# Performance work log

Measured on AMD Instinct MI355X. Metric: run time of the kernel, lower is better.

The kernel has to match this reference:

```python
import jax, jax.numpy as jnp
import numpy as np

NEG_SLOPE = 0.2  # PyG GATConv default negative_slope
HEADS1, HID = 8, 256


def gat_conv(x, src, dst, W, att_src, att_dst, bias, heads, out_ch):
    """PyG-style GATConv: project, per-edge attention, segment softmax over dst, scatter-add."""
    N = x.shape[0]
    h = (x @ W.T).reshape(N, heads, out_ch)                 # [N,H,C]
    a_s = jnp.einsum('nhc,hc->nh', h, att_src)              # [N,H]
    a_d = jnp.einsum('nhc,hc->nh', h, att_dst)
    e = jax.nn.leaky_relu(a_s[src] + a_d[dst], NEG_SLOPE)   # [E,H]
    m = jax.ops.segment_max(e, dst, num_segments=N)         # stable softmax per dst node
    ex = jnp.exp(e - m[dst])
    denom = jax.ops.segment_sum(ex, dst, num_segments=N)
    alpha = ex / (denom[dst] + 1e-16)                       # [E,H]
    out = jax.ops.segment_sum(alpha[:, :, None] * h[src], dst, num_segments=N)  # [N,H,C]
    return out.reshape(N, heads * out_ch) + bias


def setup_inputs() -> dict:
    key = jax.random.key(0)
    ks = jax.random.split(key, 20)
    Nc, Ncol, E = 4000, 16000, 100000
    nf, cf, gain, hid, H, emb = 64, 128, 2, HID, HEADS1, 128
    s = 0.05
    return {
        'constraints_state': jax.random.normal(ks[0], (Nc, nf), jnp.float32),
        'columns_state':     jax.random.normal(ks[1], (Ncol, cf), jnp.float32),
        'edges':             jax.random.randint(ks[2], (2, E), 0, Nc + Ncol, jnp.int64),
        'W_node': jax.random.normal(ks[3], (hid, nf * gain), jnp.float32) * s,
        'b_node': jnp.zeros((hid,), jnp.float32),
        'W_col':  jax.random.normal(ks[4], (hid, cf * gain), jnp.float32) * s,
        'b_col':  jnp.zeros((hid,), jnp.float32),
        'W1':       jax.random.normal(ks[5], (H * hid, hid), jnp.float32) * s,
        'att_src1': jax.random.normal(ks[6], (H, hid), jnp.float32) * s,
        'att_dst1': jax.random.normal(ks[7], (H, hid), jnp.float32) * s,
        'b1':       jnp.zeros((H * hid,), jnp.float32),
        'W2':       jax.random.normal(ks[8], (hid, H * hid), jnp.float32) * s,
        'att_src2': jax.random.normal(ks[9], (1, hid), jnp.float32) * s,
        'att_dst2': jax.random.normal(ks[10], (1, hid), jnp.float32) * s,
        'b2':       jnp.zeros((hid,), jnp.float32),
        'W_out': jax.random.normal(ks[11], (emb, hid), jnp.float32) * s,
        'b_out': jnp.zeros((emb,), jnp.float32),
    }


def reference(constraints_state, columns_state, edges,
              W_node, b_node, W_col, b_col,
              W1, att_src1, att_dst1, b1,
              W2, att_src2, att_dst2, b2,
              W_out, b_out):
    gain = 2
    x_n = jnp.tile(constraints_state, (1, gain))
    x_c = jnp.tile(columns_state, (1, gain))
    h_n = jax.nn.relu(x_n @ W_node.T + b_node)
    h_c = jax.nn.relu(x_c @ W_col.T + b_col)
    x = jnp.concatenate([h_n, h_c], axis=0)                 # [N, hid]
    N = x.shape[0]
    loops = jnp.arange(N)
    # conv1: edges as given (+ self-loops, PyG default)
    src1 = jnp.concatenate([edges[0], loops])
    dst1 = jnp.concatenate([edges[1], loops])
    x = jax.nn.relu(gat_conv(x, src1, dst1, W1, att_src1, att_dst1, b1, HEADS1, HID))
    # conv2: flipped edges (+ self-loops), 1 head
    src2 = jnp.concatenate([edges[1], loops])
    dst2 = jnp.concatenate([edges[0], loops])
    x = jax.nn.relu(gat_conv(x, src2, dst2, W2, att_src2, att_dst2, b2, 1, HID))
    logits = x[-columns_state.shape[0]:] @ W_out.T + b_out  # [Ncol, embed_dim]
    return logits
```

## Files before the change

### kernel.cpp

```cpp
#include <hip/hip_runtime.h>


#define NEG_SLOPE 0.2f

typedef __attribute__((ext_vector_type(8))) short bf16x8;
typedef __attribute__((ext_vector_type(4))) float f32x4;

__device__ __forceinline__ float bf2f(unsigned short u) {
  return __uint_as_float(((unsigned)u) << 16);
}
__device__ __forceinline__ unsigned short f2bf(float f) {
  unsigned u = __float_as_uint(f);
  u += 0x7fffu + ((u >> 16) & 1u);
  return (unsigned short)(u >> 16);
}

__device__ __forceinline__ void async_copy16(const void* g, void* l) {
  __builtin_amdgcn_global_load_lds(
      (const __attribute__((address_space(1))) unsigned int*)g,
      (__attribute__((address_space(3))) unsigned int*)l, 16, 0, 0);
}

__global__ void prep(const float* __restrict__ Wn, const float* __restrict__ Wc,
                     const float* __restrict__ W1, const float* __restrict__ W2,
                     const float* __restrict__ Wout,
                     const float* __restrict__ cons, const float* __restrict__ cols,
                     const float* __restrict__ att_s1, const float* __restrict__ att_d1,
                     unsigned short* __restrict__ Wn_b, unsigned short* __restrict__ Wc_b,
                     unsigned short* __restrict__ W1b, unsigned short* __restrict__ W2b,
                     unsigned short* __restrict__ Woutb,
                     unsigned short* __restrict__ consb, unsigned short* __restrict__ colsb,
                     float* __restrict__ v_s1, float* __restrict__ v_d1,
                     int n_cons, int n_cols) {
  const int S0 = 256 * 64;
  const int S1 = 256 * 128;
  const int S2 = 2048 * 256;
  const int S3 = 256 * 2048;
  const int S4 = 128 * 256;
  const int S5 = 2048;
  int total = S0 + S1 + S2 + S3 + S4 + n_cons + n_cols + S5;
  for (int idx = blockIdx.x * 256 + threadIdx.x; idx < total; idx += gridDim.x * 256) {
    int i = idx;
    if (i < S0) { int o = i >> 6, j = i & 63;
      Wn_b[i] = f2bf(Wn[o * 128 + j] + Wn[o * 128 + 64 + j]); continue; }
    i -= S0;
    if (i < S1) { int o = i >> 7, j = i & 127;
      Wc_b[i] = f2bf(Wc[o * 256 + j] + Wc[o * 256 + 128 + j]); continue; }
    i -= S1;
    if (i < S2) { W1b[i] = f2bf(W1[i]); continue; }
    i -= S2;
    if (i < S3) { W2b[i] = f2bf(W2[i]); continue; }
    i -= S3;
    if (i < S4) { Woutb[i] = f2bf(Wout[i]); continue; }
    i -= S4;
    if (i < n_cons) { consb[i] = f2bf(cons[i]); continue; }
    i -= n_cons;
    if (i < n_cols) { colsb[i] = f2bf(cols[i]); continue; }
    i -= n_cols;
    {
      int h = i >> 8, k = i & 255;
      const float* Wrow = W1 + (size_t)h * 256 * 256 + k;
      const float* as = att_s1 + h * 256;
      const float* ad = att_d1 + h * 256;
      float s = 0.f, d = 0.f;
      for (int c = 0; c < 256; ++c) {
        float w = Wrow[(size_t)c * 256];
        s += as[c] * w;
        d += ad[c] * w;
      }
      v_s1[i] = s; v_d1[i] = d;
    }
  }
}

__global__ __launch_bounds__(256) void a1_dots(const unsigned short* __restrict__ xb,
                                               const float* __restrict__ v_s,
                                               const float* __restrict__ v_d,
                                               float* __restrict__ a_s,
                                               float* __restrict__ a_d, int N) {
  __shared__ float vs[2048], vd[2048];
  for (int i = threadIdx.x; i < 2048; i += 256) { vs[i] = v_s[i]; vd[i] = v_d[i]; }
  __syncthreads();
  int n = blockIdx.x * 256 + threadIdx.x;
  if (n >= N) return;
  const unsigned short* row = xb + (size_t)n * 256;
  float s[8] = {}, d[8] = {};
  for (int c = 0; c < 256; c += 8) {
    bf16x8 xv = *(const bf16x8*)(row + c);
    float xf[8];
#pragma unroll
    for (int i = 0; i < 8; ++i) xf[i] = bf2f(((const unsigned short*)&xv)[i]);
#pragma unroll
    for (int h = 0; h < 8; ++h)
#pragma unroll
      for (int i = 0; i < 8; ++i) {
        s[h] += xf[i] * vs[h * 256 + c + i];
        d[h] += xf[i] * vd[h * 256 + c + i];
      }
  }
#pragma unroll
  for (int h = 0; h < 8; ++h) { a_s[n * 8 + h] = s[h]; a_d[n * 8 + h] = d[h]; }
}

__global__ __launch_bounds__(256) void a2_dots(const unsigned short* __restrict__ h2,
                                               const float* __restrict__ att_s,
                                               const float* __restrict__ att_d,
                                               float* __restrict__ a_s,
                                               float* __restrict__ a_d, int N) {
  __shared__ float ss[256], sd[256];
  if (threadIdx.x < 256) {
    ss[threadIdx.x] = att_s[threadIdx.x];
    sd[threadIdx.x] = att_d[threadIdx.x];
  }
  __syncthreads();
  int n = blockIdx.x * 256 + threadIdx.x;
  if (n >= N) return;
  const unsigned short* row = h2 + (size_t)n * 256;
  float s = 0.f, d = 0.f;
  for (int c = 0; c < 256; c += 8) {
    bf16x8 xv = *(const bf16x8*)(row + c);
#pragma unroll
    for (int i = 0; i < 8; ++i) {
      float hv = bf2f(((const unsigned short*)&xv)[i]);
      s += hv * ss[c + i];
      d += hv * sd[c + i];
    }
  }
  a_s[n] = s;
  a_d[n] = d;
}

template <bool C_BF16, bool BIAS, bool RELU, bool BDIAG, bool SWZ>
__global__ __launch_bounds__(512) void gemm_mfma_bt(const unsigned short* __restrict__ A,
                                                    const unsigned short* __restrict__ W,
                                                    const float* __restrict__ bias,
                                                    void* __restrict__ Cv,
                                                    int M, int K, int Nout, int lda) {
  __shared__ short smem[2 * 128 * 64];
  short* sA = smem;
  short* sB = smem + 128 * 64;
  float* Cf = (float*)Cv;
  unsigned short* Cb = (unsigned short*)Cv;

  const int tid = threadIdx.x;
  const int lane = tid & 63, w = tid >> 6;

  const int gx = gridDim.x;
  int wg = blockIdx.y * gx + blockIdx.x;
  if (SWZ) {
    const int nwg = gx * gridDim.y;
    int orig = wg;
    int q = nwg >> 3, r = nwg & 7;
    int xcd = orig & 7, idx = orig >> 3;
    wg = (xcd < r ? xcd * (q + 1) : r * (q + 1) + (xcd - r) * q) + idx;
  }
  const int m0 = (wg / gx) * 128, n0 = (wg % gx) * 128;

  const int koff = BDIAG ? (n0 >> 8) << 8 : 0;
  const int wm = (w & 3) * 32, wn = (w >> 2) * 64;
  const int fr = lane & 15;
  const int frs = fr & 7;
  const int quad = lane >> 4;

  f32x4 acc[2][4];
#pragma unroll
  for (int i = 0; i < 2; ++i)
#pragma unroll
    for (int j = 0; j < 4; ++j) acc[i][j] = (f32x4){0.f, 0.f, 0.f, 0.f};

  for (int k0 = 0; k0 < K; k0 += 64) {
#pragma unroll
    for (int i = 0; i < 2; ++i) {
      int c = i * 512 + tid;
      int row = c >> 3, kc = c & 7;
      int kcs = kc ^ (row & 7);
      int grow = m0 + row;
      if (grow >= M) grow = M - 1;
      async_copy16(A + (size_t)grow * lda + koff + k0 + kcs * 8, &sA[(i * 512 + w * 64) * 8]);
    }
#pragma unroll
    for (int i = 0; i < 2; ++i) {
      int c = i * 512 + tid;
      int row = c >> 3, kc = c & 7;
      int kcs = kc ^ (row & 7);
      async_copy16(W + (size_t)(n0 + row) * K + k0 + kcs * 8, &sB[(i * 512 + w * 64) * 8]);
    }
    __syncthreads();

#pragma unroll
    for (int ks = 0; ks < 2; ++ks) {
      bf16x8 af[2], bfr[4];
#pragma unroll
      for (int mi = 0; mi < 2; ++mi) {
        int row = wm + mi * 16 + fr;
        af[mi] = *(const bf16x8*)&sA[(row * 8 + ((ks * 4 + quad) ^ frs)) * 8];
      }
#pragma unroll
      for (int ni = 0; ni < 4; ++ni) {
        int row = wn + ni * 16 + fr;
        bfr[ni] = *(const bf16x8*)&sB[(row * 8 + ((ks * 4 + quad) ^ frs)) * 8];
      }
#pragma unroll
      for (int mi = 0; mi < 2; ++mi)
#pragma unroll
        for (int ni = 0; ni < 4; ++ni)
          acc[mi][ni] = __builtin_amdgcn_mfma_f32_16x16x32_bf16(
              af[mi], bfr[ni], acc[mi][ni], 0, 0, 0);
    }
    __syncthreads();
  }

  if (C_BF16) {
    unsigned short* hsh = (unsigned short*)smem;
#pragma unroll
    for (int mi = 0; mi < 2; ++mi)
#pragma unroll
      for (int ni = 0; ni < 4; ++ni) {
        int col = wn + ni * 16 + fr;
        float bv = BIAS ? bias[n0 + col] : 0.f;
        f32x4 v = acc[mi][ni];
#pragma unroll
        for (int r = 0; r < 4; ++r) {
          int row = wm + mi * 16 + quad * 4 + r;
          float x = v[r] + bv;
          if (RELU) x = fmaxf(x, 0.f);
          hsh[row * 128 + (col ^ (((row >> 2) & 3) << 5))] = f2bf(x);
        }
      }
    __syncthreads();
#pragma unroll
    for (int i = 0; i < 4; ++i) {
      int slot = i * 512 + tid;
      int row = slot >> 4, cg = slot & 15;
      int colbase = cg * 8;
      bf16x8 val = *(const bf16x8*)&hsh[row * 128 + (colbase ^ (((row >> 2) & 3) << 5))];
      int grow = m0 + row;
      if (grow < M)
        *(bf16x8*)(Cb + (size_t)grow * Nout + n0 + colbase) = val;
    }
  } else {
#pragma unroll
    for (int mi = 0; mi < 2; ++mi)
#pragma unroll
      for (int ni = 0; ni < 4; ++ni) {
        int col = n0 + wn + ni * 16 + fr;
        float bv = BIAS ? bias[col] : 0.f;
        f32x4 v = acc[mi][ni];
#pragma unroll
        for (int r = 0; r < 4; ++r) {
          int row = m0 + wm + mi * 16 + quad * 4 + r;
          if (row < M) {
            float x = v[r] + bv;
            if (RELU) x = fmaxf(x, 0.f);
            Cf[(size_t)row * Nout + col] = x;
          }
        }
      }
  }
}

__global__ void build_count(const void* __restrict__ edges_raw, int E, int N,
                            int* __restrict__ esrc, int* __restrict__ edst,
                            int* __restrict__ cnt1, int* __restrict__ cnt2, int E1) {
  const long long* p64 = (const long long*)edges_raw;
  const int* p32 = (const int*)edges_raw;
  bool is64 = true;
#pragma unroll
  for (int i = 0; i < 8; ++i) {
    long long v = p64[i];
    if (v < 0 || v >= N) is64 = false;
  }
  int idx = blockIdx.x * 256 + threadIdx.x;
  if (idx >= E1) return;
  int s, d;
  if (idx < E) {
    if (is64) { s = (int)p64[idx]; d = (int)p64[E + idx]; }
    else      { s = p32[idx];      d = p32[E + idx]; }
  } else {
    s = d = idx - E;
  }
  esrc[idx] = s;
  edst[idx] = d;
  atomicAdd(&cnt1[d], 1);
  atomicAdd(&cnt2[s], 1);
}

__device__ __forceinline__ void scan_one(const int* __restrict__ cnt,
                                         int* __restrict__ indptr,
                                         int* __restrict__ cur, int N, int* buf) {
  int t = threadIdx.x, lane = t & 63, w = t >> 6;
  int running = 0;
  for (int base = 0; base < N; base += 1024) {
    int v = (base + t < N) ? cnt[base + t] : 0;
    int incl = v;
#pragma unroll
    for (int off = 1; off < 64; off <<= 1) {
      int y = __shfl_up(incl, off);
      if (lane >= off) incl += y;
    }
    if (lane == 63) buf[w] = incl;
    __syncthreads();
    if (t < 16) {
      int x = buf[t];
#pragma unroll
      for (int off = 1; off < 16; off <<= 1) {
        int y = __shfl_up(x, off);
        if (t >= off) x += y;
      }
      buf[t] = x;
    }
    __syncthreads();
    int woff = w ? buf[w - 1] : 0;
    int tot = buf[15];
    if (base + t < N) {
      int excl = running + woff + incl - v;
      indptr[base + t] = excl;
      cur[base + t] = excl;
    }
    running += tot;
    __syncthreads();
  }
  if (t == 0) indptr[N] = running;
  __syncthreads();
}

__global__ __launch_bounds__(1024) void scan2_kernel(const int* cnt1, int* indptr1, int* cur1,
                                                     const int* cnt2, int* indptr2, int* cur2,
                                                     int N) {
  __shared__ int buf[16];
  if (blockIdx.x == 0) scan_one(cnt1, indptr1, cur1, N, buf);
  else                 scan_one(cnt2, indptr2, cur2, N, buf);
}

__global__ void scatter_edges(const int* __restrict__ esrc, const int* __restrict__ edst,
                              int* __restrict__ cur1, int* __restrict__ cur2,
                              int* __restrict__ nbr1, int* __restrict__ nbr2, int E1) {
  int e = blockIdx.x * 256 + threadIdx.x;
  if (e >= E1) return;
  int s = esrc[e], d = edst[e];
  int p1 = atomicAdd(&cur1[d], 1);
  nbr1[p1] = s;
  int p2 = atomicAdd(&cur2[s], 1);
  nbr2[p2] = d;
}

__global__ __launch_bounds__(256) void agg1_fused(const unsigned short* __restrict__ xb,
                                                  const float* __restrict__ a_s,
                                                  const float* __restrict__ a_d,
                                                  const int* __restrict__ indptr,
                                                  const int* __restrict__ nbr,
                                                  unsigned short* __restrict__ agg,
                                                  int N) {
  __shared__ float al_sh[4][64 * 8];
  const int w = threadIdx.x >> 6, lane = threadIdx.x & 63;
  const int dst = blockIdx.x * 4 + w;
  if (dst >= N) return;
  const int start = indptr[dst];
  const int deg = indptr[dst + 1] - start;
  const int c0 = lane * 4;

  float ad[8];
  *(float4*)&ad[0] = *(const float4*)&a_d[dst * 8];
  *(float4*)&ad[4] = *(const float4*)&a_d[dst * 8 + 4];

  float psum[8];
#pragma unroll
  for (int h = 0; h < 8; ++h) psum[h] = 0.f;

  float acc[8][4];
#pragma unroll
  for (int h = 0; h < 8; ++h)
#pragma unroll
    for (int i = 0; i < 4; ++i) acc[h][i] = 0.f;

  for (int base = 0; base < deg; base += 64) {
    int cnt = min(64, deg - base);
    int s = 0;
    if (lane < cnt) {
      s = nbr[start + base + lane];
      float as[8];
      *(float4*)&as[0] = *(const float4*)&a_s[s * 8];
      *(float4*)&as[4] = *(const float4*)&a_s[s * 8 + 4];
      float p8[8];
#pragma unroll
      for (int h = 0; h < 8; ++h) {
        float e = as[h] + ad[h];
        e = e > 0.f ? e : NEG_SLOPE * e;
        float pv = __expf(e);
        p8[h] = pv;
        psum[h] += pv;
      }
#pragma unroll
      for (int h = 0; h < 8; ++h) al_sh[w][lane * 8 + h] = p8[h];
    }
    __builtin_amdgcn_wave_barrier();
    for (int j = 0; j < cnt; ++j) {
      int sj = __shfl(s, j);
      f32x4 alo = *(const f32x4*)&al_sh[w][j * 8];
      f32x4 ahi = *(const f32x4*)&al_sh[w][j * 8 + 4];
      ushort4 xv = *(const ushort4*)(xb + (size_t)sj * 256 + c0);
      float x0 = bf2f(xv.x), x1 = bf2f(xv.y), x2 = bf2f(xv.z), x3 = bf2f(xv.w);
#pragma unroll
      for (int h = 0; h < 4; ++h) {
        acc[h][0] += alo[h] * x0; acc[h][1] += alo[h] * x1;
        acc[h][2] += alo[h] * x2; acc[h][3] += alo[h] * x3;
      }
#pragma unroll
      for (int h = 0; h < 4; ++h) {
        acc[h + 4][0] += ahi[h] * x0; acc[h + 4][1] += ahi[h] * x1;
        acc[h + 4][2] += ahi[h] * x2; acc[h + 4][3] += ahi[h] * x3;
      }
    }
    __builtin_amdgcn_wave_barrier();
  }

  float inv[8];
#pragma unroll
  for (int h = 0; h < 8; ++h) {
    float t = psum[h];
#pragma unroll
    for (int off = 32; off; off >>= 1) t += __shfl_xor(t, off);
    inv[h] = 1.f / (t + 1e-16f);
  }

  unsigned short* op = agg + (size_t)dst * 2048;
#pragma unroll
  for (int h = 0; h < 8; ++h) {
    unsigned short ov[4];
#pragma unroll
    for (int i = 0; i < 4; ++i) ov[i] = f2bf(acc[h][i] * inv[h]);
    *((ushort4*)(op + h * 256 + c0)) = *((const ushort4*)ov);
  }
}

__global__ __launch_bounds__(256) void agg2_fused(const unsigned short* __restrict__ h2,
                                                  const float* __restrict__ a_s,
                                                  const float* __restrict__ a_d,
                                                  const int* __restrict__ indptr,
                                                  const int* __restrict__ nbr,
                                                  const float* __restrict__ b2,
                                                  unsigned short* __restrict__ x3,
                                                  int Nc, int Ncol) {
  const int w = threadIdx.x >> 6, lane = threadIdx.x & 63;
  const int i0 = blockIdx.x * 4 + w;
  if (i0 >= Ncol) return;
  const int dst = Nc + i0;
  const int start = indptr[dst];
  const int deg = indptr[dst + 1] - start;
  const float ad = a_d[dst];
  float psum = 0.f;
  float acc[4] = {0.f, 0.f, 0.f, 0.f};
  const int c0 = lane * 4;

  for (int base = 0; base < deg; base += 64) {
    int cnt = min(64, deg - base);
    int s = 0;
    float p = 0.f;
    if (lane < cnt) {
      s = nbr[start + base + lane];
      float e = a_s[s] + ad;
      e = e > 0.f ? e : NEG_SLOPE * e;
      p = __expf(e);
      psum += p;
    }
    for (int j = 0; j < cnt; ++j) {
      int sj = __shfl(s, j);
      float al = __shfl(p, j);
      ushort4 hv = *(const ushort4*)(h2 + (size_t)sj * 256 + c0);
      acc[0] += al * bf2f(hv.x);
      acc[1] += al * bf2f(hv.y);
      acc[2] += al * bf2f(hv.z);
      acc[3] += al * bf2f(hv.w);
    }
  }

  float t = psum;
#pragma unroll
  for (int off = 32; off; off >>= 1) t += __shfl_xor(t, off);
  float inv = 1.f / (t + 1e-16f);

  float4 bv = *(const float4*)&b2[c0];
  unsigned short ov[4];
  ov[0] = f2bf(fmaxf(acc[0] * inv + bv.x, 0.f));
  ov[1] = f2bf(fmaxf(acc[1] * inv + bv.y, 0.f));
  ov[2] = f2bf(fmaxf(acc[2] * inv + bv.z, 0.f));
  ov[3] = f2bf(fmaxf(acc[3] * inv + bv.w, 0.f));
  *((ushort4*)(x3 + (size_t)i0 * 256 + c0)) = *((const ushort4*)ov);
}

extern "C" void kernel_launch(void* const* d_in, const int* in_sizes, int n_in,
                              void* d_out, int out_size, void* d_ws, size_t ws_size,
                              hipStream_t stream) {
  (void)n_in; (void)out_size; (void)ws_size;
  const float* constraints = (const float*)d_in[0];
  const float* columns     = (const float*)d_in[1];
  const void*  edges       = d_in[2];
  const float* W_node = (const float*)d_in[3];
  const float* b_node = (const float*)d_in[4];
  const float* W_col  = (const float*)d_in[5];
  const float* b_col  = (const float*)d_in[6];
  const float* W1       = (const float*)d_in[7];
  const float* att_src1 = (const float*)d_in[8];
  const float* att_dst1 = (const float*)d_in[9];
  const float* b1       = (const float*)d_in[10];
  const float* W2       = (const float*)d_in[11];
  const float* att_src2 = (const float*)d_in[12];
  const float* att_dst2 = (const float*)d_in[13];
  const float* b2       = (const float*)d_in[14];
  const float* W_out    = (const float*)d_in[15];
  const float* b_out    = (const float*)d_in[16];

  const int Nc   = in_sizes[0] / 64;
  const int Ncol = in_sizes[1] / 128;
  const int E    = in_sizes[2] / 2;
  const int N    = Nc + Ncol;
  const int E1   = E + N;

  char* p = (char*)d_ws;
  size_t off = 0;
  auto alloc = [&](size_t nbytes) -> void* {
    void* r = p + off;
    off = (off + nbytes + 255) & ~(size_t)255;
    return r;
  };
  unsigned short* Wn_b  = (unsigned short*)alloc(2ull * 256 * 64);
  unsigned short* Wc_b  = (unsigned short*)alloc(2ull * 256 * 128);
  unsigned short* W1b   = (unsigned short*)alloc(2ull * 2048 * 256);
  unsigned short* W2b   = (unsigned short*)alloc(2ull * 256 * 2048);
  unsigned short* Woutb = (unsigned short*)alloc(2ull * 128 * 256);
  unsigned short* consb = (unsigned short*)alloc(2ull * (size_t)Nc * 64);
  unsigned short* colsb = (unsigned short*)alloc(2ull * (size_t)Ncol * 128);
  unsigned short* xb    = (unsigned short*)alloc(2ull * (size_t)N * 256);
  float* v_s1 = (float*)alloc(sizeof(float) * 8 * 256);
  float* v_d1 = (float*)alloc(sizeof(float) * 8 * 256);
  float* a_s1 = (float*)alloc(sizeof(float) * (size_t)N * 8);
  float* a_d1 = (float*)alloc(sizeof(float) * (size_t)N * 8);
  int* esrc = (int*)alloc(4ull * E1);
  int* edst = (int*)alloc(4ull * E1);
  int* cnt1 = (int*)alloc(4ull * 2 * N);
  int* cnt2 = cnt1 + N;
  int* indptr1 = (int*)alloc(4ull * (N + 1));
  int* cur1    = (int*)alloc(4ull * N);
  int* indptr2 = (int*)alloc(4ull * (N + 1));
  int* cur2    = (int*)alloc(4ull * N);
  int* nbr1 = (int*)alloc(4ull * E1);
  int* nbr2 = (int*)alloc(4ull * E1);
  unsigned short* agg = (unsigned short*)alloc(2ull * (size_t)N * 2048);
  unsigned short* x2  = (unsigned short*)alloc(2ull * (size_t)N * 2048);
  unsigned short* h2b = (unsigned short*)alloc(2ull * (size_t)N * 256);
  float* a_s2 = (float*)alloc(sizeof(float) * (size_t)N);
  float* a_d2 = (float*)alloc(sizeof(float) * (size_t)N);
  unsigned short* x3 = (unsigned short*)alloc(2ull * (size_t)Ncol * 256);

  hipMemsetAsync(cnt1, 0, 4ull * 2 * N, stream);
  prep<<<1024, 256, 0, stream>>>(W_node, W_col, W1, W2, W_out, constraints, columns,
                                 att_src1, att_dst1,
                                 Wn_b, Wc_b, W1b, W2b, Woutb, consb, colsb,
                                 v_s1, v_d1, Nc * 64, Ncol * 128);

  gemm_mfma_bt<true, true, true, false, false><<<dim3(2, (Nc + 127) / 128), 512, 0, stream>>>(
      consb, Wn_b, b_node, xb, Nc, 64, 256, 64);
  gemm_mfma_bt<true, true, true, false, false><<<dim3(2, (Ncol + 127) / 128), 512, 0, stream>>>(
      colsb, Wc_b, b_col, xb + (size_t)Nc * 256, Ncol, 128, 256, 128);

  a1_dots<<<(N + 255) / 256, 256, 0, stream>>>(xb, v_s1, v_d1, a_s1, a_d1, N);

  build_count<<<(E1 + 255) / 256, 256, 0, stream>>>(edges, E, N, esrc, edst, cnt1, cnt2, E1);
  scan2_kernel<<<2, 1024, 0, stream>>>(cnt1, indptr1, cur1, cnt2, indptr2, cur2, N);
  scatter_edges<<<(E1 + 255) / 256, 256, 0, stream>>>(esrc, edst, cur1, cur2, nbr1, nbr2, E1);

  agg1_fused<<<(N + 3) / 4, 256, 0, stream>>>(xb, a_s1, a_d1, indptr1, nbr1, agg, N);
  gemm_mfma_bt<true, true, true, true, true><<<dim3(16, (N + 127) / 128), 512, 0, stream>>>(
      agg, W1b, b1, x2, N, 256, 2048, 2048);

  gemm_mfma_bt<true, false, false, false, false><<<dim3(2, (N + 127) / 128), 512, 0, stream>>>(
      x2, W2b, nullptr, h2b, N, 2048, 256, 2048);
  a2_dots<<<(N + 255) / 256, 256, 0, stream>>>(h2b, att_src2, att_dst2, a_s2, a_d2, N);
  agg2_fused<<<(Ncol + 3) / 4, 256, 0, stream>>>(h2b, a_s2, a_d2, indptr2, nbr2, b2, x3,
                                                 Nc, Ncol);

  gemm_mfma_bt<false, true, false, false, false><<<dim3(1, (Ncol + 127) / 128), 512, 0, stream>>>(
      x3, Woutb, b_out, (float*)d_out, Ncol, 256, 128, 256);
}
```

Measured before the change: 339.0 us.

## Split-K the conv2 projection GEMM with fp32 atomics and fuse bf16 conversion

The conv2 projection GEMM (K=2048, output width 256) launched only 2x157 workgroups. It now splits K four ways across blockIdx.z and atomically adds fp32 partials into a zeroed buffer. The zeroing is folded into the existing memset, and a2_dots now reads the fp32 result, writes the bf16 copy, and computes the attention dots from the rounded values. This trades more parallelism on a long-K GEMM for fp32 atomic traffic, a larger memset, and non-deterministic summation order.

```diff
diff --git a/kernel.cpp b/kernel.cpp
--- a/kernel.cpp
+++ b/kernel.cpp
@@ -102,7 +102,8 @@
   for (int h = 0; h < 8; ++h) { a_s[n * 8 + h] = s[h]; a_d[n * 8 + h] = d[h]; }
 }
 
-__global__ __launch_bounds__(256) void a2_dots(const unsigned short* __restrict__ h2,
+__global__ __launch_bounds__(256) void a2_dots(const float* __restrict__ h2f,
+                                               unsigned short* __restrict__ h2b,
                                                const float* __restrict__ att_s,
                                                const float* __restrict__ att_d,
                                                float* __restrict__ a_s,
@@ -115,22 +116,24 @@
   __syncthreads();
   int n = blockIdx.x * 256 + threadIdx.x;
   if (n >= N) return;
-  const unsigned short* row = h2 + (size_t)n * 256;
+  const float* row = h2f + (size_t)n * 256;
+  unsigned short* orow = h2b + (size_t)n * 256;
   float s = 0.f, d = 0.f;
-  for (int c = 0; c < 256; c += 8) {
-    bf16x8 xv = *(const bf16x8*)(row + c);
-#pragma unroll
-    for (int i = 0; i < 8; ++i) {
-      float hv = bf2f(((const unsigned short*)&xv)[i]);
-      s += hv * ss[c + i];
-      d += hv * sd[c + i];
-    }
+  for (int c = 0; c < 256; c += 4) {
+    float4 xv = *(const float4*)(row + c);
+    unsigned short ov[4];
+    ov[0] = f2bf(xv.x); ov[1] = f2bf(xv.y); ov[2] = f2bf(xv.z); ov[3] = f2bf(xv.w);
+    *(ushort4*)(orow + c) = *(const ushort4*)ov;
+    s += bf2f(ov[0]) * ss[c] + bf2f(ov[1]) * ss[c + 1] +
+         bf2f(ov[2]) * ss[c + 2] + bf2f(ov[3]) * ss[c + 3];
+    d += bf2f(ov[0]) * sd[c] + bf2f(ov[1]) * sd[c + 1] +
+         bf2f(ov[2]) * sd[c + 2] + bf2f(ov[3]) * sd[c + 3];
   }
   a_s[n] = s;
   a_d[n] = d;
 }
 
-template <bool C_BF16, bool BIAS, bool RELU, bool BDIAG, bool SWZ>
+template <bool C_BF16, bool BIAS, bool RELU, bool BDIAG, bool SWZ, int SK>
 __global__ __launch_bounds__(512) void gemm_mfma_bt(const unsigned short* __restrict__ A,
                                                     const unsigned short* __restrict__ W,
                                                     const float* __restrict__ bias,
@@ -157,6 +160,8 @@
   const int m0 = (wg / gx) * 128, n0 = (wg % gx) * 128;
 
   const int koff = BDIAG ? (n0 >> 8) << 8 : 0;
+  const int kspan = K / SK;
+  const int kbeg = (SK > 1) ? blockIdx.z * kspan : 0;
   const int wm = (w & 3) * 32, wn = (w >> 2) * 64;
   const int fr = lane & 15;
   const int frs = fr & 7;
@@ -168,7 +173,7 @@
 #pragma unroll
     for (int j = 0; j < 4; ++j) acc[i][j] = (f32x4){0.f, 0.f, 0.f, 0.f};
 
-  for (int k0 = 0; k0 < K; k0 += 64) {
+  for (int k0 = kbeg; k0 < kbeg + kspan; k0 += 64) {
 #pragma unroll
     for (int i = 0; i < 2; ++i) {
       int c = i * 512 + tid;
@@ -250,9 +255,13 @@
         for (int r = 0; r < 4; ++r) {
           int row = m0 + wm + mi * 16 + quad * 4 + r;
           if (row < M) {
-            float x = v[r] + bv;
-            if (RELU) x = fmaxf(x, 0.f);
-            Cf[(size_t)row * Nout + col] = x;
+            if (SK > 1) {
+              atomicAdd(&Cf[(size_t)row * Nout + col], v[r]);
+            } else {
+              float x = v[r] + bv;
+              if (RELU) x = fmaxf(x, 0.f);
+              Cf[(size_t)row * Nout + col] = x;
+            }
           }
         }
       }
@@ -535,10 +544,15 @@
   float* v_d1 = (float*)alloc(sizeof(float) * 8 * 256);
   float* a_s1 = (float*)alloc(sizeof(float) * (size_t)N * 8);
   float* a_d1 = (float*)alloc(sizeof(float) * (size_t)N * 8);
+
+  size_t zoff0 = off;
+  int* cnt1 = (int*)alloc(4ull * 2 * N);
+  int* cnt2 = cnt1 + N;
+  float* h2f = (float*)alloc(sizeof(float) * (size_t)N * 256);
+  size_t zbytes = off - zoff0;
+
   int* esrc = (int*)alloc(4ull * E1);
   int* edst = (int*)alloc(4ull * E1);
-  int* cnt1 = (int*)alloc(4ull * 2 * N);
-  int* cnt2 = cnt1 + N;
   int* indptr1 = (int*)alloc(4ull * (N + 1));
   int* cur1    = (int*)alloc(4ull * N);
   int* indptr2 = (int*)alloc(4ull * (N + 1));
@@ -552,15 +566,15 @@
   float* a_d2 = (float*)alloc(sizeof(float) * (size_t)N);
   unsigned short* x3 = (unsigned short*)alloc(2ull * (size_t)Ncol * 256);
 
-  hipMemsetAsync(cnt1, 0, 4ull * 2 * N, stream);
+  hipMemsetAsync(cnt1, 0, zbytes, stream);
   prep<<<1024, 256, 0, stream>>>(W_node, W_col, W1, W2, W_out, constraints, columns,
                                  att_src1, att_dst1,
                                  Wn_b, Wc_b, W1b, W2b, Woutb, consb, colsb,
                                  v_s1, v_d1, Nc * 64, Ncol * 128);
 
-  gemm_mfma_bt<true, true, true, false, false><<<dim3(2, (Nc + 127) / 128), 512, 0, stream>>>(
+  gemm_mfma_bt<true, true, true, false, false, 1><<<dim3(2, (Nc + 127) / 128), 512, 0, stream>>>(
       consb, Wn_b, b_node, xb, Nc, 64, 256, 64);
-  gemm_mfma_bt<true, true, true, false, false><<<dim3(2, (Ncol + 127) / 128), 512, 0, stream>>>(
+  gemm_mfma_bt<true, true, true, false, false, 1><<<dim3(2, (Ncol + 127) / 128), 512, 0, stream>>>(
       colsb, Wc_b, b_col, xb + (size_t)Nc * 256, Ncol, 128, 256, 128);
 
   a1_dots<<<(N + 255) / 256, 256, 0, stream>>>(xb, v_s1, v_d1, a_s1, a_d1, N);
@@ -570,15 +584,15 @@
   scatter_edges<<<(E1 + 255) / 256, 256, 0, stream>>>(esrc, edst, cur1, cur2, nbr1, nbr2, E1);
 
   agg1_fused<<<(N + 3) / 4, 256, 0, stream>>>(xb, a_s1, a_d1, indptr1, nbr1, agg, N);
-  gemm_mfma_bt<true, true, true, true, true><<<dim3(16, (N + 127) / 128), 512, 0, stream>>>(
+  gemm_mfma_bt<true, true, true, true, true, 1><<<dim3(16, (N + 127) / 128), 512, 0, stream>>>(
       agg, W1b, b1, x2, N, 256, 2048, 2048);
 
-  gemm_mfma_bt<true, false, false, false, false><<<dim3(2, (N + 127) / 128), 512, 0, stream>>>(
-      x2, W2b, nullptr, h2b, N, 2048, 256, 2048);
-  a2_dots<<<(N + 255) / 256, 256, 0, stream>>>(h2b, att_src2, att_dst2, a_s2, a_d2, N);
+  gemm_mfma_bt<false, false, false, false, false, 4><<<dim3(2, (N + 127) / 128, 4), 512, 0, stream>>>(
+      x2, W2b, nullptr, h2f, N, 2048, 256, 2048);
+  a2_dots<<<(N + 255) / 256, 256, 0, stream>>>(h2f, h2b, att_src2, att_dst2, a_s2, a_d2, N);
   agg2_fused<<<(Ncol + 3) / 4, 256, 0, stream>>>(h2b, a_s2, a_d2, indptr2, nbr2, b2, x3,
                                                  Nc, Ncol);
 
-  gemm_mfma_bt<false, true, false, false, false><<<dim3(1, (Ncol + 127) / 128), 512, 0, stream>>>(
+  gemm_mfma_bt<false, true, false, false, false, 1><<<dim3(1, (Ncol + 127) / 128), 512, 0, stream>>>(
       x3, Woutb, b_out, (float*)d_out, Ncol, 256, 128, 256);
 }
```

Result: slower. 391.8 us (+15.6%).
